# Performance work log

Measured on AMD Instinct MI355X. Metric: run time of the kernel, lower is better.

The kernel has to match this reference:

```python
import jax, jax.numpy as jnp
import numpy as np

N = 8192        # args.network_verNum (nodes)
T = 6           # args.pick_T_num (snapshots)
STEP = 3        # timesteps between consecutive picks


def setup_inputs() -> dict:
    key = jax.random.key(0)
    k1, k2, k3 = jax.random.split(key, 3)
    # adjacency mask (~avg degree 16) and IC-style edge probabilities, as in reset_parameters
    adj = jax.random.uniform(k1, (N, N)) < 0.002
    vals = jnp.array([0.03, 0.05, 0.07, 0.1, 0.12], dtype=jnp.float32)
    idx = jax.random.randint(k2, (N, N), 0, 5)
    weight = jnp.where(adj, vals[idx], 0.0).astype(jnp.float32)
    # monotone 0/1 activation snapshots [T, N]
    snaps = (jax.random.uniform(k3, (T, N)) < 0.05).astype(jnp.float32)
    snaps = jnp.clip(jnp.cumsum(snaps, axis=0), 0.0, 1.0)
    time_pick = np.arange(T, dtype=np.int64) * STEP
    return {"snapshot_vec_series": snaps, "weight": weight, "time_pick": time_pick}


def reference(snapshot_vec_series, weight, time_pick):
    # snapshot_vec_series: [T, N] float; weight: [N, N] float; time_pick: [T] static ints
    tp = np.asarray(time_pick)
    Tn = snapshot_vec_series.shape[0]

    def step(rv, _):
        # P2[i, j] = weight[j, i] * rv[j]; neg_mul[i] = prod_j (1 - P2[i, j])
        neg_mul = jnp.prod(1.0 - weight * rv[:, None], axis=0)  # [N]
        return 1.0 - neg_mul, None

    outs = []
    for T_index in range(1, Tn - 1):
        rv = snapshot_vec_series[T_index] - snapshot_vec_series[T_index - 1]  # newly activated
        n_steps = int(tp[T_index + 1] - tp[T_index])
        rv, _ = jax.lax.scan(step, rv, None, length=n_steps)
        outs.append(rv)
    return jnp.stack(outs)  # [T-2, N]
```

## Files before the change

kernel.cpp:

```cpp
#include <hip/hip_runtime.h>
#include <hip/hip_bf16.h>


#define CAP  64
#define QMAX 128

typedef float floatx4 __attribute__((ext_vector_type(4)));

template <bool POW2>
__global__ __launch_bounds__(256) void build_edges_kernel(
    const floatx4* __restrict__ W4, unsigned total4, unsigned log2N, unsigned maskN,
    int* __restrict__ cnt, uint2* __restrict__ epk, unsigned N) {
    __shared__ unsigned qcount;
    __shared__ unsigned qw[QMAX];
    __shared__ unsigned qji[QMAX];
    if (threadIdx.x == 0) qcount = 0u;
    __syncthreads();

    const unsigned gsize = gridDim.x * blockDim.x;
    unsigned e4 = blockIdx.x * blockDim.x + threadIdx.x;

    auto emit = [&](float w, unsigned j, unsigned i) {
        unsigned k = atomicAdd(&qcount, 1u);
        if (k < QMAX) {
            qw[k]  = __float_as_uint(w);
            qji[k] = (j << 16) | i;
        } else {
            int s = atomicAdd(&cnt[i], 1);
            if (s < CAP) { uint2 p; p.x = __float_as_uint(w); p.y = j;
                           epk[(unsigned)s * N + i] = p; }
        }
    };
    auto process = [&](floatx4 v, unsigned e) {
        unsigned ored = __float_as_uint(v.x) | __float_as_uint(v.y) |
                        __float_as_uint(v.z) | __float_as_uint(v.w);
        if (ored == 0u) return;
        unsigned j, i0;
        if (POW2) { j = e >> log2N; i0 = e & maskN; }
        else      { j = e / N;      i0 = e - j * N; }
#pragma unroll
        for (int t = 0; t < 4; ++t)
            if (v[t] != 0.0f) emit(v[t], j, i0 + t);
    };

    for (; e4 + 3u * gsize < total4; e4 += 4u * gsize) {
        floatx4 v0 = W4[e4];
        floatx4 v1 = W4[e4 + gsize];
        floatx4 v2 = W4[e4 + 2u * gsize];
        floatx4 v3 = W4[e4 + 3u * gsize];
        process(v0, (e4) << 2);
        process(v1, (e4 + gsize) << 2);
        process(v2, (e4 + 2u * gsize) << 2);
        process(v3, (e4 + 3u * gsize) << 2);
    }
    for (; e4 < total4; e4 += gsize) process(W4[e4], e4 << 2);

    __syncthreads();
    unsigned qn = qcount < (unsigned)QMAX ? qcount : (unsigned)QMAX;
    for (unsigned t = threadIdx.x; t < qn; t += blockDim.x) {
        unsigned wbits = qw[t], ji = qji[t];
        unsigned i = ji & 0xffffu, j = ji >> 16;
        int s = atomicAdd(&cnt[i], 1);
        if (s < CAP) { uint2 p; p.x = wbits; p.y = j;
                       epk[(unsigned)s * N + i] = p; }
    }
}

template <bool FIRST>
__global__ __launch_bounds__(256) void step_lp_kernel(
    const float* __restrict__ rv_in,
    const float* __restrict__ snaps,
    float* __restrict__ rv_out,
    const int* __restrict__ cnt,
    const uint2* __restrict__ epk,
    int N) {
    const int c    = blockIdx.y;
    const int lane = threadIdx.x & 31;
    const int grp  = threadIdx.x >> 5;
    const int i    = blockIdx.x * 8 + grp;
    if (i >= N) return;
    const float* rv = rv_in + (size_t)c * N;
    const float* sa = snaps + (size_t)(c + 1) * N;
    const float* sb = snaps + (size_t)c * N;
    int n = cnt[i];
    if (n > CAP) n = CAP;
    float prod = 1.0f;
    for (int k = lane; k < n; k += 32) {
        uint2 p = epk[(size_t)k * N + i];
        float w = __uint_as_float(p.x);
        int j = (int)p.y;
        float r = FIRST ? (sa[j] - sb[j]) : rv[j];
        prod *= 1.0f - w * r;
    }
    for (int off = 16; off; off >>= 1) prod *= __shfl_xor(prod, off, 32);
    if (lane == 0) rv_out[(size_t)c * N + i] = 1.0f - prod;
}

extern "C" void kernel_launch(void* const* d_in, const int* in_sizes, int n_in,
                              void* d_out, int out_size, void* d_ws, size_t ws_size,
                              hipStream_t stream) {
    const float* snaps = (const float*)d_in[0];
    const float* W     = (const float*)d_in[1];

    const int T = in_sizes[2];
    const int N = in_sizes[0] / T;
    const int chains = T - 2;
    const int NSTEPS = 3;

    char* ws = (char*)d_ws;
    int*   cnt = (int*)ws;
    size_t off = ((size_t)N * 4 + 255) & ~(size_t)255;
    float* rvA = (float*)(ws + off);
    off += ((size_t)chains * N * 4 + 255) & ~(size_t)255;
    float* rvB = (float*)(ws + off);
    off += ((size_t)chains * N * 4 + 255) & ~(size_t)255;
    uint2* epk = (uint2*)(ws + off);

    hipMemsetAsync(cnt, 0, (size_t)N * sizeof(int), stream);

    const unsigned total4 = (unsigned)((size_t)N * N / 4);
    const bool pow2 = (N & (N - 1)) == 0;
    unsigned log2N = 0;
    while ((1u << log2N) < (unsigned)N) ++log2N;
    const int bblk = 256;
    int bgrd = (int)((total4 + (unsigned)bblk * 16 - 1) / ((unsigned)bblk * 16));
    if (bgrd < 1) bgrd = 1;
    if (pow2)
        build_edges_kernel<true><<<bgrd, bblk, 0, stream>>>(
            (const floatx4*)W, total4, log2N, (unsigned)N - 1, cnt, epk, (unsigned)N);
    else
        build_edges_kernel<false><<<bgrd, bblk, 0, stream>>>(
            (const floatx4*)W, total4, log2N, (unsigned)N - 1, cnt, epk, (unsigned)N);

    dim3 sgrd((N + 7) / 8, chains);
    float* outp = (float*)d_out;

    float* out0 = (NSTEPS == 1) ? outp : rvA;
    step_lp_kernel<true><<<sgrd, 256, 0, stream>>>(nullptr, snaps, out0, cnt, epk, N);
    float* bufs[2] = {rvA, rvB};
    for (int s = 1; s < NSTEPS; ++s) {
        const float* in = bufs[(s - 1) & 1];
        float* out = (s == NSTEPS - 1) ? outp : bufs[s & 1];
        step_lp_kernel<false><<<sgrd, 256, 0, stream>>>(in, nullptr, out, cnt, epk, N);
    }
}
```

Baseline: 70.83 us.

## Fuse propagation steps into one shared-memory kernel per chain, unroll edge build

Replaces the three per-step launches with a single kernel per chain. It keeps the activation vector in shared memory across steps and syncs within the block instead of between launches. The build kernel is unrolled 8-way with a larger shared queue and half as many blocks. Only a handful of blocks are used, so the edge gathers become latency bound on a few CUs.

```diff
diff --git a/kernel.cpp b/kernel.cpp
--- a/kernel.cpp
+++ b/kernel.cpp
@@ -3,7 +3,7 @@
 
 
 #define CAP  64
-#define QMAX 128
+#define QMAX 256
 
 typedef float floatx4 __attribute__((ext_vector_type(4)));
 
@@ -43,15 +43,23 @@
             if (v[t] != 0.0f) emit(v[t], j, i0 + t);
     };
 
-    for (; e4 + 3u * gsize < total4; e4 += 4u * gsize) {
+    for (; e4 + 7u * gsize < total4; e4 += 8u * gsize) {
         floatx4 v0 = W4[e4];
         floatx4 v1 = W4[e4 + gsize];
         floatx4 v2 = W4[e4 + 2u * gsize];
         floatx4 v3 = W4[e4 + 3u * gsize];
+        floatx4 v4 = W4[e4 + 4u * gsize];
+        floatx4 v5 = W4[e4 + 5u * gsize];
+        floatx4 v6 = W4[e4 + 6u * gsize];
+        floatx4 v7 = W4[e4 + 7u * gsize];
         process(v0, (e4) << 2);
         process(v1, (e4 + gsize) << 2);
         process(v2, (e4 + 2u * gsize) << 2);
         process(v3, (e4 + 3u * gsize) << 2);
+        process(v4, (e4 + 4u * gsize) << 2);
+        process(v5, (e4 + 5u * gsize) << 2);
+        process(v6, (e4 + 6u * gsize) << 2);
+        process(v7, (e4 + 7u * gsize) << 2);
     }
     for (; e4 < total4; e4 += gsize) process(W4[e4], e4 << 2);
 
@@ -66,14 +74,69 @@
     }
 }
 
+#define NMAX 8192
+template <int CPT>
+__global__ __launch_bounds__(1024) void steps_fused_kernel(
+    const float* __restrict__ snaps,
+    float* __restrict__ out,
+    const int* __restrict__ cnt,
+    const uint2* __restrict__ epk,
+    int N, int nsteps) {
+    __shared__ float rvbuf[2][NMAX];
+    const int c = blockIdx.x;
+    const int tid = threadIdx.x;
+    const int nthr = blockDim.x;
+
+    const floatx4* sa4 = (const floatx4*)(snaps + (size_t)(c + 1) * N);
+    const floatx4* sb4 = (const floatx4*)(snaps + (size_t)c * N);
+    floatx4* r04 = (floatx4*)rvbuf[0];
+    for (int t = tid; t < N / 4; t += nthr) r04[t] = sa4[t] - sb4[t];
+
+    int nn[CPT];
+#pragma unroll
+    for (int u = 0; u < CPT; ++u) {
+        int i = tid + u * nthr;
+        int n = cnt[i];
+        nn[u] = n > CAP ? CAP : n;
+    }
+    __syncthreads();
+
+    int cur = 0;
+    for (int s = 0; s < nsteps; ++s) {
+        const float* rv = rvbuf[cur];
+        float* rn = rvbuf[cur ^ 1];
+#pragma unroll
+        for (int u = 0; u < CPT; ++u) {
+            int i = tid + u * nthr;
+            int n = nn[u];
+            float pa = 1.0f, pb = 1.0f;
+            int k = 0;
+            for (; k + 1 < n; k += 2) {
+                uint2 p0 = epk[(size_t)k * N + i];
+                uint2 p1 = epk[(size_t)(k + 1) * N + i];
+                pa *= 1.0f - __uint_as_float(p0.x) * rv[(int)p0.y];
+                pb *= 1.0f - __uint_as_float(p1.x) * rv[(int)p1.y];
+            }
+            if (k < n) {
+                uint2 p0 = epk[(size_t)k * N + i];
+                pa *= 1.0f - __uint_as_float(p0.x) * rv[(int)p0.y];
+            }
+            rn[i] = 1.0f - pa * pb;
+        }
+        __syncthreads();
+        cur ^= 1;
+    }
+
+    const floatx4* rc4 = (const floatx4*)rvbuf[cur];
+    floatx4* o4 = (floatx4*)(out + (size_t)c * N);
+    for (int t = tid; t < N / 4; t += nthr) o4[t] = rc4[t];
+}
+
 template <bool FIRST>
 __global__ __launch_bounds__(256) void step_lp_kernel(
-    const float* __restrict__ rv_in,
-    const float* __restrict__ snaps,
-    float* __restrict__ rv_out,
-    const int* __restrict__ cnt,
-    const uint2* __restrict__ epk,
-    int N) {
+    const float* __restrict__ rv_in, const float* __restrict__ snaps,
+    float* __restrict__ rv_out, const int* __restrict__ cnt,
+    const uint2* __restrict__ epk, int N) {
     const int c    = blockIdx.y;
     const int lane = threadIdx.x & 31;
     const int grp  = threadIdx.x >> 5;
@@ -87,10 +150,8 @@
     float prod = 1.0f;
     for (int k = lane; k < n; k += 32) {
         uint2 p = epk[(size_t)k * N + i];
-        float w = __uint_as_float(p.x);
-        int j = (int)p.y;
-        float r = FIRST ? (sa[j] - sb[j]) : rv[j];
-        prod *= 1.0f - w * r;
+        float r = FIRST ? (sa[(int)p.y] - sb[(int)p.y]) : rv[(int)p.y];
+        prod *= 1.0f - __uint_as_float(p.x) * r;
     }
     for (int off = 16; off; off >>= 1) prod *= __shfl_xor(prod, off, 32);
     if (lane == 0) rv_out[(size_t)c * N + i] = 1.0f - prod;
@@ -123,7 +184,7 @@
     unsigned log2N = 0;
     while ((1u << log2N) < (unsigned)N) ++log2N;
     const int bblk = 256;
-    int bgrd = (int)((total4 + (unsigned)bblk * 16 - 1) / ((unsigned)bblk * 16));
+    int bgrd = (int)((total4 + (unsigned)bblk * 32 - 1) / ((unsigned)bblk * 32));
     if (bgrd < 1) bgrd = 1;
     if (pow2)
         build_edges_kernel<true><<<bgrd, bblk, 0, stream>>>(
@@ -132,15 +193,19 @@
         build_edges_kernel<false><<<bgrd, bblk, 0, stream>>>(
             (const floatx4*)W, total4, log2N, (unsigned)N - 1, cnt, epk, (unsigned)N);
 
-    dim3 sgrd((N + 7) / 8, chains);
     float* outp = (float*)d_out;
-
-    float* out0 = (NSTEPS == 1) ? outp : rvA;
-    step_lp_kernel<true><<<sgrd, 256, 0, stream>>>(nullptr, snaps, out0, cnt, epk, N);
-    float* bufs[2] = {rvA, rvB};
-    for (int s = 1; s < NSTEPS; ++s) {
-        const float* in = bufs[(s - 1) & 1];
-        float* out = (s == NSTEPS - 1) ? outp : bufs[s & 1];
-        step_lp_kernel<false><<<sgrd, 256, 0, stream>>>(in, nullptr, out, cnt, epk, N);
-    }
-}
+    if (N == 8192) {
+        steps_fused_kernel<8><<<chains, 1024, 0, stream>>>(
+            snaps, outp, cnt, epk, N, NSTEPS);
+    } else {
+        dim3 sgrd((N + 7) / 8, chains);
+        float* out0 = (NSTEPS == 1) ? outp : rvA;
+        step_lp_kernel<true><<<sgrd, 256, 0, stream>>>(nullptr, snaps, out0, cnt, epk, N);
+        float* bufs[2] = {rvA, rvB};
+        for (int s = 1; s < NSTEPS; ++s) {
+            const float* in = bufs[(s - 1) & 1];
+            float* out = (s == NSTEPS - 1) ? outp : bufs[s & 1];
+            step_lp_kernel<false><<<sgrd, 256, 0, stream>>>(in, nullptr, out, cnt, epk, N);
+        }
+    }
+}
```

After: 149.4 us. 2.11x slower.

## Store edges row-contiguous per node and process all four chains per node group

Applied to the files above, without the earlier changes.

Edge storage moves from slot-major (s*N+i) to node-major (i*CAP+s), so each node's incoming edges sit contiguously. A new step kernel assigns a 16-lane group to each (node, chain) pair and fuses all four chains into one 1D grid, so the edge list for a node is read by adjacent groups and stays in cache. The build kernel's shared-memory queue also grows to 256 entries to cut global atomic spills. The trade-off is that the build kernel's scattered writes now stride by CAP per node, and fewer lanes work per node.

```diff
diff --git a/kernel.cpp b/kernel.cpp
--- a/kernel.cpp
+++ b/kernel.cpp
@@ -3,7 +3,7 @@
 
 
 #define CAP  64
-#define QMAX 128
+#define QMAX 256
 
 typedef float floatx4 __attribute__((ext_vector_type(4)));
 
@@ -28,7 +28,7 @@
         } else {
             int s = atomicAdd(&cnt[i], 1);
             if (s < CAP) { uint2 p; p.x = __float_as_uint(w); p.y = j;
-                           epk[(unsigned)s * N + i] = p; }
+                           epk[(size_t)i * CAP + s] = p; }
         }
     };
     auto process = [&](floatx4 v, unsigned e) {
@@ -62,22 +62,48 @@
         unsigned i = ji & 0xffffu, j = ji >> 16;
         int s = atomicAdd(&cnt[i], 1);
         if (s < CAP) { uint2 p; p.x = wbits; p.y = j;
-                       epk[(unsigned)s * N + i] = p; }
+                       epk[(size_t)i * CAP + s] = p; }
     }
 }
 
 template <bool FIRST>
-__global__ __launch_bounds__(256) void step_lp_kernel(
+__global__ __launch_bounds__(256) void step_csr_kernel(
     const float* __restrict__ rv_in,
     const float* __restrict__ snaps,
     float* __restrict__ rv_out,
     const int* __restrict__ cnt,
     const uint2* __restrict__ epk,
     int N) {
+    const int lane = threadIdx.x & 15;
+    const int g    = blockIdx.x * 16 + (threadIdx.x >> 4);
+    const int i    = g >> 2;
+    const int c    = g & 3;
+    if (i >= N) return;
+    const float* rv = rv_in + (size_t)c * N;
+    const float* sa = snaps + (size_t)(c + 1) * N;
+    const float* sb = snaps + (size_t)c * N;
+    int n = cnt[i];
+    if (n > CAP) n = CAP;
+    float prod = 1.0f;
+    for (int k = lane; k < n; k += 16) {
+        uint2 p = epk[(size_t)i * CAP + k];
+        float w = __uint_as_float(p.x);
+        int j = (int)p.y;
+        float r = FIRST ? (sa[j] - sb[j]) : rv[j];
+        prod *= 1.0f - w * r;
+    }
+    for (int off = 8; off; off >>= 1) prod *= __shfl_xor(prod, off, 16);
+    if (lane == 0) rv_out[(size_t)c * N + i] = 1.0f - prod;
+}
+
+template <bool FIRST>
+__global__ __launch_bounds__(256) void step_lp_kernel(
+    const float* __restrict__ rv_in, const float* __restrict__ snaps,
+    float* __restrict__ rv_out, const int* __restrict__ cnt,
+    const uint2* __restrict__ epk, int N) {
     const int c    = blockIdx.y;
     const int lane = threadIdx.x & 31;
-    const int grp  = threadIdx.x >> 5;
-    const int i    = blockIdx.x * 8 + grp;
+    const int i    = blockIdx.x * 8 + (threadIdx.x >> 5);
     if (i >= N) return;
     const float* rv = rv_in + (size_t)c * N;
     const float* sa = snaps + (size_t)(c + 1) * N;
@@ -86,11 +112,9 @@
     if (n > CAP) n = CAP;
     float prod = 1.0f;
     for (int k = lane; k < n; k += 32) {
-        uint2 p = epk[(size_t)k * N + i];
-        float w = __uint_as_float(p.x);
-        int j = (int)p.y;
-        float r = FIRST ? (sa[j] - sb[j]) : rv[j];
-        prod *= 1.0f - w * r;
+        uint2 p = epk[(size_t)i * CAP + k];
+        float r = FIRST ? (sa[(int)p.y] - sb[(int)p.y]) : rv[(int)p.y];
+        prod *= 1.0f - __uint_as_float(p.x) * r;
     }
     for (int off = 16; off; off >>= 1) prod *= __shfl_xor(prod, off, 32);
     if (lane == 0) rv_out[(size_t)c * N + i] = 1.0f - prod;
@@ -132,15 +156,25 @@
         build_edges_kernel<false><<<bgrd, bblk, 0, stream>>>(
             (const floatx4*)W, total4, log2N, (unsigned)N - 1, cnt, epk, (unsigned)N);
 
-    dim3 sgrd((N + 7) / 8, chains);
     float* outp = (float*)d_out;
-
-    float* out0 = (NSTEPS == 1) ? outp : rvA;
-    step_lp_kernel<true><<<sgrd, 256, 0, stream>>>(nullptr, snaps, out0, cnt, epk, N);
     float* bufs[2] = {rvA, rvB};
-    for (int s = 1; s < NSTEPS; ++s) {
-        const float* in = bufs[(s - 1) & 1];
-        float* out = (s == NSTEPS - 1) ? outp : bufs[s & 1];
-        step_lp_kernel<false><<<sgrd, 256, 0, stream>>>(in, nullptr, out, cnt, epk, N);
+    if (chains == 4) {
+        int blocks = (N * 4 + 15) / 16;
+        float* out0 = (NSTEPS == 1) ? outp : rvA;
+        step_csr_kernel<true><<<blocks, 256, 0, stream>>>(nullptr, snaps, out0, cnt, epk, N);
+        for (int s = 1; s < NSTEPS; ++s) {
+            const float* in = bufs[(s - 1) & 1];
+            float* out = (s == NSTEPS - 1) ? outp : bufs[s & 1];
+            step_csr_kernel<false><<<blocks, 256, 0, stream>>>(in, nullptr, out, cnt, epk, N);
+        }
+    } else {
+        dim3 sgrd((N + 7) / 8, chains);
+        float* out0 = (NSTEPS == 1) ? outp : rvA;
+        step_lp_kernel<true><<<sgrd, 256, 0, stream>>>(nullptr, snaps, out0, cnt, epk, N);
+        for (int s = 1; s < NSTEPS; ++s) {
+            const float* in = bufs[(s - 1) & 1];
+            float* out = (s == NSTEPS - 1) ? outp : bufs[s & 1];
+            step_lp_kernel<false><<<sgrd, 256, 0, stream>>>(in, nullptr, out, cnt, epk, N);
+        }
     }
 }
```

Measured after the change: 70.29 us. About the same (-0.8%).
